# Performance work log

Measured on AMD Instinct MI355X. Metric: run time of the kernel, lower is better.

The kernel has to match this reference:

```python
import jax, jax.numpy as jnp
import numpy as np

T, N, D, E, O = 2, 4096, 1024, 8, 1024

def setup_inputs() -> dict:
    key = jax.random.key(0)
    k1, k2, k3 = jax.random.split(key, 3)
    x = jax.random.normal(k1, (T, N, D), dtype=jnp.float32)
    Wg = jax.random.normal(k2, (T, D, E), dtype=jnp.float32) * (1.0 / np.sqrt(D))
    We = jax.random.normal(k3, (E, D, O), dtype=jnp.float32) * (1.0 / np.sqrt(D))
    return {"x": x, "Wg": Wg, "We": We, "k": 2}


def reference(x, Wg, We, k):
    # Per-task gating logits: [T, N, E]
    logits = jnp.einsum('tnd,tde->tne', x, Wg)
    # Top-k mask per token (scatter 1.0 at top-k indices)
    _, topk_idx = jax.lax.top_k(logits, k)                      # [T, N, k]
    mask = jax.nn.one_hot(topk_idx, E, dtype=logits.dtype).sum(-2)  # [T, N, E]
    masked = mask * logits
    gates = masked / (masked.sum(-1, keepdims=True) + 1e-9)     # [T, N, E]
    # Dense expert outputs (each expert is Linear(D, O)): [T, N, E, O]
    eout = jnp.einsum('tnd,edo->tneo', x, We)
    # Weighted combine over selected experts
    out = jnp.einsum('tne,tneo->tno', gates, eout)              # [T, N, O]
    return out
```

## Files before the change

kernel.cpp:

```cpp
#include <hip/hip_runtime.h>
#include <hip/hip_bf16.h>
#include <stdint.h>

#define T_ 2
#define N_ 4096
#define D_ 1024
#define E_ 8
#define O_ 1024

#define BM 128
#define BN 128
#define BK 32

typedef __attribute__((ext_vector_type(8))) short short8;
typedef __attribute__((ext_vector_type(4))) float f32x4;

#define AS1 __attribute__((address_space(1)))
#define AS3 __attribute__((address_space(3)))

__device__ inline void gld16(const unsigned short* g, unsigned short* l) {
    __builtin_amdgcn_global_load_lds((const AS1 unsigned int*)g,
                                     (AS3 unsigned int*)l, 16, 0, 0);
}

__device__ inline unsigned short f2bf(float f) {
    union { float f; unsigned u; } v; v.f = f;
    unsigned r = v.u + 0x7fff + ((v.u >> 16) & 1);
    return (unsigned short)(r >> 16);
}

__global__ __launch_bounds__(256) void prep_kernel(
    const float* __restrict__ x, const float* __restrict__ Wg,
    const float* __restrict__ We,
    unsigned short* __restrict__ xb, unsigned short* __restrict__ Wbp,
    int* __restrict__ route, float2* __restrict__ gpair)
{
    __shared__ __align__(16) char smem[E_ * D_ * 4];
    int tid = threadIdx.x;

    if (blockIdx.x < 1024) {
        float (*WgT)[D_] = (float(*)[D_])smem;
        int wave = tid >> 6, lane = tid & 63;
        int token0 = blockIdx.x * 8;
        int t = token0 >> 12;
        const float* wgb = Wg + (size_t)t * D_ * E_;

#pragma unroll
        for (int r = 0; r < 8; ++r) {
            int f = r * 1024 + tid * 4;
            float4 v = *(const float4*)(wgb + f);
            WgT[f & 7][f >> 3]             = v.x;
            WgT[(f + 1) & 7][(f + 1) >> 3] = v.y;
            WgT[(f + 2) & 7][(f + 2) >> 3] = v.z;
            WgT[(f + 3) & 7][(f + 3) >> 3] = v.w;
        }
        __syncthreads();

#pragma unroll
        for (int tl = 0; tl < 2; ++tl) {
            int token = token0 + wave * 2 + tl;
            const float* xrow = x + (size_t)token * D_;

            float4 xv[4];
#pragma unroll
            for (int c = 0; c < 4; ++c)
                xv[c] = *(const float4*)(xrow + c * 256 + lane * 4);

            float acc[E_] = {0.f, 0.f, 0.f, 0.f, 0.f, 0.f, 0.f, 0.f};
#pragma unroll
            for (int c = 0; c < 4; ++c) {
                int d0 = c * 256 + lane * 4;
                unsigned lo = f2bf(xv[c].x) | ((unsigned)f2bf(xv[c].y) << 16);
                unsigned hi = f2bf(xv[c].z) | ((unsigned)f2bf(xv[c].w) << 16);
                *(uint2*)(&xb[(size_t)token * D_ + d0]) = make_uint2(lo, hi);
#pragma unroll
                for (int e = 0; e < E_; ++e) {
                    float4 w = *(const float4*)(&WgT[e][d0]);
                    acc[e] += xv[c].x * w.x + xv[c].y * w.y + xv[c].z * w.z + xv[c].w * w.w;
                }
            }
#pragma unroll
            for (int off = 1; off < 64; off <<= 1) {
#pragma unroll
                for (int e = 0; e < E_; ++e) acc[e] += __shfl_xor(acc[e], off, 64);
            }

            if (lane == 0) {
                float best = acc[0]; int bi = 0;
#pragma unroll
                for (int e = 1; e < E_; ++e) if (acc[e] > best) { best = acc[e]; bi = e; }
                float sec = -INFINITY; int si = 0;
#pragma unroll
                for (int e = 0; e < E_; ++e) if (e != bi && acc[e] > sec) { sec = acc[e]; si = e; }
                float s = best + sec + 1e-9f;
                route[token] = bi | (si << 8);
                gpair[token] = make_float2(best / s, sec / s);
            }
        }
    } else {
        unsigned short* P = (unsigned short*)smem;

        int b = blockIdx.x - 1024;
        int e  = b >> 7;
        int oy = (b & 127) >> 3;
        int dz = b & 7;
        int o0 = oy * 64, d0 = dz * 128;

#pragma unroll
        for (int r = 0; r < 32; ++r) {
            int lin = r * 256 + tid;
            int dd = lin >> 6, oo = lin & 63;
            P[oo * 136 + dd] = f2bf(We[((size_t)(e * D_ + d0 + dd)) * O_ + o0 + oo]);
        }
        __syncthreads();

#pragma unroll
        for (int w = 0; w < 4; ++w) {
            int ci   = w * 256 + tid;
            int lane = ci & 63;
            int c16  = (ci >> 6) & 3;
            int ks   = ci >> 8;
            int fr = lane & 15, q = lane >> 4;
            uint4 v = *(const uint4*)&P[(c16 * 16 + fr) * 136 + ks * 32 + q * 8];
            int ot  = oy >> 1;
            int cb  = (oy * 4 + c16) & 7;
            int ksa = dz * 4 + ks;
            size_t idx = ((((size_t)(e * 8 + ot) * 32 + ksa) * 8 + cb) * 64 + lane) * 8;
            *(uint4*)(Wbp + idx) = v;
        }
    }
}

__global__ __launch_bounds__(1024) void build_lists(
    const int* __restrict__ route, const float2* __restrict__ gpair,
    int* __restrict__ toklist, float* __restrict__ gatelist,
    int* __restrict__ counts)
{
    int g = blockIdx.x;
    int t = g >> 3, e = g & 7;
    int tid = threadIdx.x;
    int wave = tid >> 6, lane = tid & 63;

    __shared__ int waveSum[16];
    __shared__ int base;
    if (tid == 0) base = 0;

    for (int c = 0; c < N_; c += 1024) {
        int n = c + tid;
        int r = route[t * N_ + n];
        int e0 = r & 255, e1 = (r >> 8) & 255;
        bool sel = (e0 == e) || (e1 == e);
        unsigned long long b = __ballot(sel);
        int pre  = __popcll(b & ((1ull << lane) - 1ull));
        if (lane == 0) waveSum[wave] = __popcll(b);
        __syncthreads();
        int woff = 0, total = 0;
#pragma unroll
        for (int w = 0; w < 16; ++w) {
            int s = waveSum[w];
            total += s;
            woff += (w < wave) ? s : 0;
        }
        if (sel) {
            int p = base + woff + pre;
            int slot = (e0 == e) ? 0 : 1;
            toklist[g * N_ + p] = n | (slot << 16);
            float2 gp = gpair[t * N_ + n];
            gatelist[g * N_ + p] = (e0 == e) ? gp.x : gp.y;
        }
        __syncthreads();
        if (tid == 0) base += total;
    }
    __syncthreads();
    if (tid == 0) counts[g] = base;
}

__global__ __launch_bounds__(512, 4) void moe_gemm(
    const unsigned short* __restrict__ xb,
    const unsigned short* __restrict__ Wbp,
    const int* __restrict__ toklist, const float* __restrict__ gatelist,
    const int* __restrict__ counts, float* __restrict__ out)
{
    int lin = blockIdx.x;
    int mt  = lin >> 7;
    int u   = lin & 127;
    int xcd = u & 7;
    int v   = u >> 3;
    int g   = 2 * xcd + (v >> 3);
    int ot  = v & 7;
    int t   = g >> 3;

    int cnt = counts[g];
    int m0 = mt * BM;
    if (m0 >= cnt) return;

    __shared__ __align__(16) unsigned short As[2][BM * BK];
    __shared__ int   tokS[BM];
    __shared__ float gateS[BM];

    int tid = threadIdx.x;
    if (tid < BM) {
        int r = m0 + tid;
        tokS[tid]  = (r < cnt) ? toklist[g * N_ + r]  : -1;
        gateS[tid] = (r < cnt) ? gatelist[g * N_ + r] : 0.f;
    }
    __syncthreads();

    int wave = tid >> 6, lane = tid & 63;
    int lr = lane >> 2;
    int sg = (lane & 3) ^ ((lane >> 3) & 3);
    int ar = wave * 16 + lr;
    int tok = max(tokS[ar], 0) & 0xFFFF;
    const unsigned short* ag = xb + ((size_t)(t * N_ + tok)) * D_ + sg * 8;

    const unsigned short* wf =
        Wbp + ((size_t)((g & 7) * 8 + ot) * 32) * 4096;
    int cb0 = (wave >> 1) * 2;
    const unsigned short* bp0 = wf + cb0 * 512 + lane * 8;
    const unsigned short* bp1 = bp0 + 512;

    int fr = lane & 15, q = lane >> 4;
    int wm = (wave & 1) * 64;
    int wn = (wave >> 1) * 32;
    int fp = (q ^ ((fr >> 1) & 3)) * 8;

    f32x4 acc[4][2];
#pragma unroll
    for (int mi = 0; mi < 4; ++mi)
#pragma unroll
        for (int ni = 0; ni < 2; ++ni) acc[mi][ni] = (f32x4){0.f, 0.f, 0.f, 0.f};

    short8 bf0[2], bf1[2];

    gld16(ag, &As[0][wave * 512]);
    asm volatile("" ::: "memory");
    bf0[0] = *(const short8*)(bp0);
    bf0[1] = *(const short8*)(bp1);

#define KSTEP(CUR, NXT, BC, BNX, IT)                                           \
    {                                                                          \
        asm volatile("s_waitcnt vmcnt(2)" ::: "memory");     \
        __builtin_amdgcn_s_barrier();                                          \
        asm volatile("" ::: "memory");       \
        int kk = (IT) + 1;                                                     \
        if (kk < D_ / BK) {                                                    \
            gld16(ag + (size_t)kk * BK, &As[NXT][wave * 512]);                 \
            asm volatile("" ::: "memory");     \
            BNX[0] = *(const short8*)(bp0 + (size_t)kk * 4096);                \
            BNX[1] = *(const short8*)(bp1 + (size_t)kk * 4096);                \
        }                                                                      \
        short8 af[4];                                                          \
        _Pragma("unroll") for (int mi = 0; mi < 4; ++mi)                       \
            af[mi] = *(const short8*)(&As[CUR][(wm + mi * 16 + fr) * BK + fp]);\
        _Pragma("unroll") for (int mi = 0; mi < 4; ++mi) {                     \
            acc[mi][0] = __builtin_amdgcn_mfma_f32_16x16x32_bf16(              \
                af[mi], BC[0], acc[mi][0], 0, 0, 0);                           \
            acc[mi][1] = __builtin_amdgcn_mfma_f32_16x16x32_bf16(              \
                af[mi], BC[1], acc[mi][1], 0, 0, 0);                           \
        }                                                                      \
    }

    for (int it = 0; it < D_ / BK; it += 2) {
        KSTEP(0, 1, bf0, bf1, it)
        KSTEP(1, 0, bf1, bf0, it + 1)
    }
#undef KSTEP

    float* outb = out + (size_t)t * N_ * O_;
    int ncol = ot * 128 + wn + fr;
#pragma unroll
    for (int mi = 0; mi < 4; ++mi) {
#pragma unroll
        for (int r = 0; r < 4; ++r) {
            int ml = wm + mi * 16 + q * 4 + r;
            int ent = tokS[ml];
            if (ent >= 0) {
                int tokk = ent & 0xFFFF;
                int slot = ent >> 16;
                float gate = gateS[ml];
#pragma unroll
                for (int ni = 0; ni < 2; ++ni) {
                    unsigned short* p =
                        (unsigned short*)(outb + (size_t)tokk * O_ + ncol + ni * 16);
                    p[slot] = f2bf(gate * acc[mi][ni][r]);
                }
            }
        }
    }
}

__global__ __launch_bounds__(256) void combine_kernel(float* __restrict__ out)
{
    size_t i = ((size_t)blockIdx.x * 256 + threadIdx.x) * 4;
    unsigned* po = (unsigned*)out;
    uint4 v = *(uint4*)(po + i);
    float4 r;
    union { unsigned u; float f; } a, b;
#define CMB(comp, src) a.u = (src) << 16; b.u = (src) & 0xFFFF0000u; comp = a.f + b.f
    CMB(r.x, v.x); CMB(r.y, v.y); CMB(r.z, v.z); CMB(r.w, v.w);
#undef CMB
    *(float4*)(out + i) = r;
}

extern "C" void kernel_launch(void* const* d_in, const int* in_sizes, int n_in,
                              void* d_out, int out_size, void* d_ws, size_t ws_size,
                              hipStream_t stream)
{
    const float* x  = (const float*)d_in[0];
    const float* Wg = (const float*)d_in[1];
    const float* We = (const float*)d_in[2];
    float* out = (float*)d_out;

    char* ws = (char*)d_ws;
    unsigned short* xb   = (unsigned short*)(ws);
    unsigned short* Wbp  = (unsigned short*)(ws + 16777216);
    int*   toklist       = (int*)  (ws + 33554432);
    float* gatelist      = (float*)(ws + 33816576);
    int*   counts        = (int*)  (ws + 34078720);
    int*   route         = (int*)  (ws + 34078976);
    float2* gpair        = (float2*)(ws + 34111744);

    prep_kernel<<<2048, 256, 0, stream>>>(x, Wg, We, xb, Wbp, route, gpair);
    build_lists<<<T_ * E_, 1024, 0, stream>>>(route, gpair, toklist, gatelist, counts);
    moe_gemm<<<(N_ / BM) * 8 * (T_ * E_), 512, 0, stream>>>(
        xb, Wbp, toklist, gatelist, counts, out);
    combine_kernel<<<((size_t)T_ * N_ * O_) / (256 * 4), 256, 0, stream>>>(out);
}
```

Baseline: 177.5 us.

## Stage A in four-k-slice rounds with deeper B prefetch and MFMA priority

Restructures the grouped-GEMM main loop so each barrier covers four BK slices of A, loaded via global_load_lds into a larger double-buffered LDS array. B fragments are prefetched up to four slices ahead in registers. MFMA blocks are wrapped in s_setprio. The goal is fewer barriers per K and more latency hiding. In exchange, LDS use per block grows fourfold and register pressure rises, which may reduce occupancy. The vmcnt accounting also becomes harder to get right.

```diff
diff --git a/kernel.cpp b/kernel.cpp
--- a/kernel.cpp
+++ b/kernel.cpp
@@ -194,7 +194,7 @@
     int m0 = mt * BM;
     if (m0 >= cnt) return;
 
-    __shared__ __align__(16) unsigned short As[2][BM * BK];
+    __shared__ __align__(16) unsigned short As[2][4][BM * BK];
     __shared__ int   tokS[BM];
     __shared__ float gateS[BM];
 
@@ -230,41 +230,70 @@
 #pragma unroll
         for (int ni = 0; ni < 2; ++ni) acc[mi][ni] = (f32x4){0.f, 0.f, 0.f, 0.f};
 
-    short8 bf0[2], bf1[2];
-
-    gld16(ag, &As[0][wave * 512]);
-    asm volatile("" ::: "memory");
-    bf0[0] = *(const short8*)(bp0);
-    bf0[1] = *(const short8*)(bp1);
-
-#define KSTEP(CUR, NXT, BC, BNX, IT)                                           \
+    short8 b0[2], b1[2], b2[2], b3[2];
+
+#define LDB(DST, K)                                                            \
     {                                                                          \
-        asm volatile("s_waitcnt vmcnt(2)" ::: "memory");     \
-        __builtin_amdgcn_s_barrier();                                          \
-        asm volatile("" ::: "memory");       \
-        int kk = (IT) + 1;                                                     \
-        if (kk < D_ / BK) {                                                    \
-            gld16(ag + (size_t)kk * BK, &As[NXT][wave * 512]);                 \
-            asm volatile("" ::: "memory");     \
-            BNX[0] = *(const short8*)(bp0 + (size_t)kk * 4096);                \
-            BNX[1] = *(const short8*)(bp1 + (size_t)kk * 4096);                \
-        }                                                                      \
+        size_t kc_ = (size_t)((K) < 31 ? (K) : 31);   \
+        DST[0] = *(const short8*)(bp0 + kc_ * 4096);                           \
+        DST[1] = *(const short8*)(bp1 + kc_ * 4096);                           \
+    }
+
+#define STAGEQ(BUF, R)                                                         \
+    {                                                                          \
+        gld16(ag + (size_t)((R) * 4 + 0) * BK, &As[BUF][0][wave * 512]);       \
+        gld16(ag + (size_t)((R) * 4 + 1) * BK, &As[BUF][1][wave * 512]);       \
+        gld16(ag + (size_t)((R) * 4 + 2) * BK, &As[BUF][2][wave * 512]);       \
+        gld16(ag + (size_t)((R) * 4 + 3) * BK, &As[BUF][3][wave * 512]);       \
+    }
+
+#define STEP(CUR, J, BC)                                                       \
+    {                                                                          \
         short8 af[4];                                                          \
         _Pragma("unroll") for (int mi = 0; mi < 4; ++mi)                       \
-            af[mi] = *(const short8*)(&As[CUR][(wm + mi * 16 + fr) * BK + fp]);\
+            af[mi] = *(const short8*)(                                         \
+                &As[CUR][J][(wm + mi * 16 + fr) * BK + fp]);                   \
+        __builtin_amdgcn_s_setprio(1);                                         \
         _Pragma("unroll") for (int mi = 0; mi < 4; ++mi) {                     \
             acc[mi][0] = __builtin_amdgcn_mfma_f32_16x16x32_bf16(              \
                 af[mi], BC[0], acc[mi][0], 0, 0, 0);                           \
             acc[mi][1] = __builtin_amdgcn_mfma_f32_16x16x32_bf16(              \
                 af[mi], BC[1], acc[mi][1], 0, 0, 0);                           \
         }                                                                      \
-    }
-
-    for (int it = 0; it < D_ / BK; it += 2) {
-        KSTEP(0, 1, bf0, bf1, it)
-        KSTEP(1, 0, bf1, bf0, it + 1)
-    }
-#undef KSTEP
+        __builtin_amdgcn_s_setprio(0);                                         \
+    }
+
+    STAGEQ(0, 0)
+    asm volatile("" ::: "memory");
+    LDB(b0, 0)
+    LDB(b1, 1)
+
+#define ROUND(CUR, NXT, R)                                                     \
+    {                                                                          \
+        asm volatile("s_waitcnt vmcnt(4)" ::: "memory");      \
+        __builtin_amdgcn_s_barrier();                                          \
+        asm volatile("" ::: "memory");       \
+        LDB(b2, (R) * 4 + 2)                 \
+        LDB(b3, (R) * 4 + 3)                                                   \
+        asm volatile("" ::: "memory");                                         \
+        if ((R) + 1 < 8) STAGEQ(NXT, (R) + 1)                                  \
+        asm volatile("" ::: "memory");       \
+        STEP(CUR, 0, b0)                                                       \
+        LDB(b0, (R) * 4 + 4)                     \
+        STEP(CUR, 1, b1)                                                       \
+        LDB(b1, (R) * 4 + 5)                                                   \
+        STEP(CUR, 2, b2)                                                       \
+        STEP(CUR, 3, b3)                                                       \
+    }
+
+    for (int r = 0; r < 8; r += 2) {
+        ROUND(0, 1, r)
+        ROUND(1, 0, r + 1)
+    }
+#undef ROUND
+#undef STEP
+#undef STAGEQ
+#undef LDB
 
     float* outb = out + (size_t)t * N_ * O_;
     int ncol = ot * 128 + wn + fr;
```

Result: slower. 182.8 us (+3.0%).

## Replace bf16 slot-pair combine pass with fp32 atomic accumulation and single-pass list build

Applied to the files above, without the earlier changes.

Drops the separate combine kernel. Extra prep blocks now zero the fp32 output, and the GEMM epilogue adds gated results into it with unsafeAtomicAdd instead of writing two bf16 halves per output word. build_lists also goes from a four-chunk loop with barriers to one pass where each thread handles four tokens and a shuffle-based wave prefix scan assigns positions. This removes one full read-write pass over the 32MB output and keeps fp32 precision in the combine. In exchange it adds 32MB of zeroing writes plus atomic traffic in the GEMM epilogue.

```diff
diff --git a/kernel.cpp b/kernel.cpp
--- a/kernel.cpp
+++ b/kernel.cpp
@@ -33,10 +33,19 @@
     const float* __restrict__ x, const float* __restrict__ Wg,
     const float* __restrict__ We,
     unsigned short* __restrict__ xb, unsigned short* __restrict__ Wbp,
-    int* __restrict__ route, float2* __restrict__ gpair)
+    int* __restrict__ route, float2* __restrict__ gpair,
+    float* __restrict__ out)
 {
     __shared__ __align__(16) char smem[E_ * D_ * 4];
     int tid = threadIdx.x;
+
+    if (blockIdx.x >= 2048) {
+        float4 z = {0.f, 0.f, 0.f, 0.f};
+        float4* dst = (float4*)out + (size_t)(blockIdx.x - 2048) * 1024;
+#pragma unroll
+        for (int k = 0; k < 4; ++k) dst[k * 256 + tid] = z;
+        return;
+    }
 
     if (blockIdx.x < 1024) {
         float (*WgT)[D_] = (float(*)[D_])smem;
@@ -142,37 +151,44 @@
     int wave = tid >> 6, lane = tid & 63;
 
     __shared__ int waveSum[16];
-    __shared__ int base;
-    if (tid == 0) base = 0;
-
-    for (int c = 0; c < N_; c += 1024) {
-        int n = c + tid;
-        int r = route[t * N_ + n];
-        int e0 = r & 255, e1 = (r >> 8) & 255;
-        bool sel = (e0 == e) || (e1 == e);
-        unsigned long long b = __ballot(sel);
-        int pre  = __popcll(b & ((1ull << lane) - 1ull));
-        if (lane == 0) waveSum[wave] = __popcll(b);
-        __syncthreads();
-        int woff = 0, total = 0;
-#pragma unroll
-        for (int w = 0; w < 16; ++w) {
-            int s = waveSum[w];
-            total += s;
-            woff += (w < wave) ? s : 0;
-        }
-        if (sel) {
-            int p = base + woff + pre;
-            int slot = (e0 == e) ? 0 : 1;
-            toklist[g * N_ + p] = n | (slot << 16);
+
+    int4 r4 = *(const int4*)(route + t * N_ + tid * 4);
+    int rr[4] = {r4.x, r4.y, r4.z, r4.w};
+    int sel[4], slot[4], mycnt = 0;
+#pragma unroll
+    for (int j = 0; j < 4; ++j) {
+        int e0 = rr[j] & 255, e1 = (rr[j] >> 8) & 255;
+        sel[j]  = (e0 == e) || (e1 == e);
+        slot[j] = (e0 == e) ? 0 : 1;
+        mycnt  += sel[j];
+    }
+    int x = mycnt;
+#pragma unroll
+    for (int off = 1; off < 64; off <<= 1) {
+        int y = __shfl_up(x, off, 64);
+        if (lane >= off) x += y;
+    }
+    if (lane == 63) waveSum[wave] = x;
+    __syncthreads();
+    int woff = 0, total = 0;
+#pragma unroll
+    for (int w = 0; w < 16; ++w) {
+        int s = waveSum[w];
+        total += s;
+        woff += (w < wave) ? s : 0;
+    }
+    int p = woff + x - mycnt;
+#pragma unroll
+    for (int j = 0; j < 4; ++j) {
+        if (sel[j]) {
+            int n = tid * 4 + j;
+            toklist[g * N_ + p] = n | (slot[j] << 16);
             float2 gp = gpair[t * N_ + n];
-            gatelist[g * N_ + p] = (e0 == e) ? gp.x : gp.y;
-        }
-        __syncthreads();
-        if (tid == 0) base += total;
-    }
-    __syncthreads();
-    if (tid == 0) counts[g] = base;
+            gatelist[g * N_ + p] = (slot[j] == 0) ? gp.x : gp.y;
+            ++p;
+        }
+    }
+    if (tid == 0) counts[g] = total;
 }
 
 __global__ __launch_bounds__(512, 4) void moe_gemm(
@@ -276,30 +292,14 @@
             int ent = tokS[ml];
             if (ent >= 0) {
                 int tokk = ent & 0xFFFF;
-                int slot = ent >> 16;
                 float gate = gateS[ml];
-#pragma unroll
-                for (int ni = 0; ni < 2; ++ni) {
-                    unsigned short* p =
-                        (unsigned short*)(outb + (size_t)tokk * O_ + ncol + ni * 16);
-                    p[slot] = f2bf(gate * acc[mi][ni][r]);
-                }
+                float* orow = outb + (size_t)tokk * O_ + ncol;
+#pragma unroll
+                for (int ni = 0; ni < 2; ++ni)
+                    unsafeAtomicAdd(orow + ni * 16, gate * acc[mi][ni][r]);
             }
         }
     }
-}
-
-__global__ __launch_bounds__(256) void combine_kernel(float* __restrict__ out)
-{
-    size_t i = ((size_t)blockIdx.x * 256 + threadIdx.x) * 4;
-    unsigned* po = (unsigned*)out;
-    uint4 v = *(uint4*)(po + i);
-    float4 r;
-    union { unsigned u; float f; } a, b;
-#define CMB(comp, src) a.u = (src) << 16; b.u = (src) & 0xFFFF0000u; comp = a.f + b.f
-    CMB(r.x, v.x); CMB(r.y, v.y); CMB(r.z, v.z); CMB(r.w, v.w);
-#undef CMB
-    *(float4*)(out + i) = r;
 }
 
 extern "C" void kernel_launch(void* const* d_in, const int* in_sizes, int n_in,
@@ -320,9 +320,8 @@
     int*   route         = (int*)  (ws + 34078976);
     float2* gpair        = (float2*)(ws + 34111744);
 
-    prep_kernel<<<2048, 256, 0, stream>>>(x, Wg, We, xb, Wbp, route, gpair);
+    prep_kernel<<<4096, 256, 0, stream>>>(x, Wg, We, xb, Wbp, route, gpair, out);
     build_lists<<<T_ * E_, 1024, 0, stream>>>(route, gpair, toklist, gatelist, counts);
     moe_gemm<<<(N_ / BM) * 8 * (T_ * E_), 512, 0, stream>>>(
         xb, Wbp, toklist, gatelist, counts, out);
-    combine_kernel<<<((size_t)T_ * N_ * O_) / (256 * 4), 256, 0, stream>>>(out);
-}
+}
```

New measurement: 198.3 us. 11.7% more time.
